# Kernel optimization log

Measured on AMD Instinct MI355X. Metric: run time of the kernel, lower is better.

The kernel has to match this reference:

```python
import jax, jax.numpy as jnp
import numpy as np

N = 100000   # nodes
D = 64       # input_dim
R = 16       # supprot (num relations)
NB = 8       # num_base
H = 128      # h_dim
E = 3200000  # edges (avg degree 32)


def setup_inputs() -> dict:
    key = jax.random.key(0)
    ks = jax.random.split(key, 7)
    vertex = jax.random.normal(ks[0], (N, D), dtype=jnp.float32)
    edge_src = jax.random.randint(ks[1], (E,), 0, N)
    edge_dst = jax.random.randint(ks[2], (E,), 0, N)
    edge_rel = jax.random.randint(ks[3], (E,), 0, R)
    edge_val = jax.random.uniform(ks[4], (E,), dtype=jnp.float32)
    W = jax.random.normal(ks[5], (D * NB, H), dtype=jnp.float32) * 0.05
    W_comp = jax.random.normal(ks[6], (R, NB), dtype=jnp.float32) * 0.3
    B = jnp.zeros((H,), dtype=jnp.float32)
    return {"vertex": vertex, "edge_val": edge_val, "W": W, "W_comp": W_comp,
            "B": B, "edge_src": edge_src, "edge_dst": edge_dst, "edge_rel": edge_rel}


def reference(vertex, edge_val, W, W_comp, B, edge_src, edge_dst, edge_rel):
    # per-relation spmm: supports[:, r*D:(r+1)*D] = A_r @ vertex (relation-major concat)
    msg = edge_val[:, None] * vertex[edge_src]              # [E, D]
    seg = edge_dst * R + edge_rel                            # combined (node, relation) segment
    supports = jax.ops.segment_sum(msg, seg, num_segments=N * R)  # [N*R, D]
    supports = supports.reshape(N, R * D)                    # [N, R*D]
    # basis decomposition (faithful to original reshape/permute ordering)
    Wr = W.reshape(NB, D, H).transpose(1, 0, 2)              # [D, NB, H]
    V = jnp.einsum('rb,dbh->drh', W_comp, Wr).reshape(D * R, H)  # [D*R, H]
    return supports @ V + B
```

## Files before the change

kernel.cpp:

```cpp
#include <hip/hip_runtime.h>
#include <hip/hip_bf16.h>
#include <stdint.h>

#define N_NODES 100000
#define DIM     64
#define NRELS   16
#define NBASE   8
#define HDIM    128
#define NEDGE   3200000
#define KDIM    1024

#define CBSH    8
#define CBN     256
#define NCB     391
#define BCAP    9216
#define SEGPB   (CBN * NRELS)
#define REC_PAD 256
#define NOFS_STRIDE 257

#define P1_BLOCKS 500
#define P1_EPT    25

#define PRO_VEFF_BLKS 512
#define PRO_VTXB_BLKS 12500
#define PRO_BLKS (PRO_VEFF_BLKS + PRO_VTXB_BLKS + 2)

typedef __attribute__((ext_vector_type(8))) short  short8;
typedef __attribute__((ext_vector_type(4))) float  f32x4;

#define OFF_VEFF  0u
#define OFF_VTXB  262144u
#define OFF_BCUR  13062144u
#define OFF_NOFS  13064192u
#define OFF_REC1  13473792u
#define REC_BYTES ((size_t)(NCB * BCAP + REC_PAD) * 8u)
#define OFF_REC2  (13473792u + REC_BYTES)
#define WS_NEED   (OFF_REC2 + REC_BYTES)

static __device__ __forceinline__ unsigned short f2bf(float x) {
    union { float f; unsigned u; } t; t.f = x;
    unsigned u = t.u;
    unsigned r = u + 0x7FFFu + ((u >> 16) & 1u);
    return (unsigned short)(r >> 16);
}

__global__ __launch_bounds__(256) void prologue(
        const float* __restrict__ W, const float* __restrict__ Wc,
        __hip_bfloat16* __restrict__ veff,
        const float* __restrict__ vert, unsigned* __restrict__ vb,
        int* __restrict__ bcur) {
    int b = blockIdx.x, t = threadIdx.x;
    if (b < PRO_VEFF_BLKS) {
        int idx = b * 256 + t;
        int c = idx >> 7;
        int h = idx & 127;
        float acc = 0.f;
#pragma unroll
        for (int bb = 0; bb < NBASE; ++bb)
            acc += Wc[(c & 15) * NBASE + bb] * W[(bb * DIM + (c >> 4)) * HDIM + h];
        int kt = c >> 5, ko = c & 31;
        int lane = ((ko >> 3) << 4) | (h & 15);
        int j = ko & 7;
        int hb = h >> 4;
        ((unsigned short*)veff)[(size_t)((kt * 8 + hb) * 64 + lane) * 8 + j] = f2bf(acc);
    } else if (b < PRO_VEFF_BLKS + PRO_VTXB_BLKS) {
        int i = (b - PRO_VEFF_BLKS) * 256 + t;
        float2 f = ((const float2*)vert)[i];
        unsigned r;
        asm("v_cvt_pk_bf16_f32 %0, %1, %2" : "=v"(r) : "v"(f.x), "v"(f.y));
        vb[i] = r;
    } else {
        int i = (b - PRO_VEFF_BLKS - PRO_VTXB_BLKS) * 256 + t;
        if (i < NCB) bcur[i] = i * BCAP;
    }
}

__global__ __launch_bounds__(256) void pass1_scatter(
        const int* __restrict__ esrc, const int* __restrict__ edst,
        const int* __restrict__ erel, const float* __restrict__ eval,
        int* __restrict__ bcur, uint2* __restrict__ recs1) {
    __shared__ int lcnt[NCB], lbase[NCB];
    int t = threadIdx.x;
    int base = blockIdx.x * (256 * P1_EPT);
    for (int i = t; i < NCB; i += 256) lcnt[i] = 0;
    __syncthreads();
#pragma unroll 5
    for (int k = 0; k < P1_EPT; ++k)
        atomicAdd(&lcnt[edst[base + k * 256 + t] >> CBSH], 1);
    __syncthreads();
    for (int i = t; i < NCB; i += 256) {
        int c = lcnt[i];
        if (c > 0) lbase[i] = atomicAdd(&bcur[i], c);
        lcnt[i] = 0;
    }
    __syncthreads();
#pragma unroll 5
    for (int k = 0; k < P1_EPT; ++k) {
        int e = base + k * 256 + t;
        int dst = edst[e];
        int cb = dst >> CBSH;
        int slot = atomicAdd(&lcnt[cb], 1);
        uint2 r;
        r.x = (unsigned)esrc[e] | ((unsigned)erel[e] << 17)
            | ((unsigned)(dst & (CBN - 1)) << 21);
        r.y = __float_as_uint(eval[e]);
        recs1[lbase[cb] + slot] = r;
    }
}

__global__ __launch_bounds__(256) void pass2_scatter(
        const uint2* __restrict__ recs1, const int* __restrict__ bcur,
        int* __restrict__ nofs, uint2* __restrict__ recs2) {
    __shared__ int cur[SEGPB];
    __shared__ int wsum[4];
    int t = threadIdx.x;
    int cb = blockIdx.x;
    int r0 = cb * BCAP;
    int r1 = bcur[cb];
    int rend = r0 + BCAP; if (r1 > rend) r1 = rend;
    for (int i = t; i < SEGPB; i += 256) cur[i] = 0;
    __syncthreads();
    for (int i = r0 + t; i < r1; i += 256) {
        unsigned rx = recs1[i].x;
        int lseg = (int)(((rx >> 21) & 255u) * 16u + ((rx >> 17) & 15u));
        atomicAdd(&cur[lseg], 1);
    }
    __syncthreads();
    int b0 = t * 16;
    int vals[16]; int tsum = 0;
#pragma unroll
    for (int k = 0; k < 16; ++k) { vals[k] = cur[b0 + k]; tsum += vals[k]; }
    int lane = t & 63, w = t >> 6;
    int x = tsum;
#pragma unroll
    for (int d = 1; d < 64; d <<= 1) { int y = __shfl_up(x, d); if (lane >= d) x += y; }
    if (lane == 63) wsum[w] = x;
    __syncthreads();
    int wadd = 0;
    for (int i = 0; i < w; ++i) wadd += wsum[i];
    int run = r0 + wadd + x - tsum;
    nofs[cb * NOFS_STRIDE + t] = run;
#pragma unroll
    for (int k = 0; k < 16; ++k) { cur[b0 + k] = run; run += vals[k]; }
    if (t == 255) nofs[cb * NOFS_STRIDE + 256] = run;
    __syncthreads();
    for (int i = r0 + t; i < r1; i += 256) {
        uint2 r = recs1[i];
        int lseg = (int)(((r.x >> 21) & 255u) * 16u + ((r.x >> 17) & 15u));
        int pos = atomicAdd(&cur[lseg], 1);
        recs2[pos] = r;
    }
}

__global__ __launch_bounds__(512, 4) void fused_agg_gemm(
        const unsigned short* __restrict__ vtxb, const uint2* __restrict__ recs,
        const int* __restrict__ nofs, const __hip_bfloat16* __restrict__ veff,
        const float* __restrict__ bias, float* __restrict__ out) {
    __shared__ __align__(16) unsigned char smem[33 * 2048];
    int t = threadIdx.x;
    int g = blockIdx.x;
    int w = t >> 6, lane = t & 63;
    int q = lane >> 4, p = lane & 15;
    int nloc = w * 4 + q;
    int n = g * 32 + nloc;

    for (int i = t; i < 33 * 2048 / 16; i += 512)
        ((uint4*)smem)[i] = make_uint4(0, 0, 0, 0);
    __syncthreads();

    int cbn = n >> CBSH, lo = n & (CBN - 1);
    int e0 = nofs[cbn * NOFS_STRIDE + lo];
    int e1 = nofs[cbn * NOFS_STRIDE + lo + 1];

    unsigned rowb2 = (unsigned)nloc * 2048u
                   + ((unsigned)(p * 8) ^ ((unsigned)(nloc & 7) << 4));
    unsigned scrb2 = 32u * 2048u + (unsigned)(p * 8);

    f32x4 acc = (f32x4)0.f;
    int currel = -1;
    const uint2* vtx2 = (const uint2*)vtxb;

    uint2 r0, r1, r2, r3, r4, r5, r6, r7;
    r0 = recs[e0 + 0]; r1 = recs[e0 + 1]; r2 = recs[e0 + 2]; r3 = recs[e0 + 3];
    r4 = recs[e0 + 4]; r5 = recs[e0 + 5]; r6 = recs[e0 + 6]; r7 = recs[e0 + 7];

    for (int base = e0; __any(base < e1); base += 8) {
        uint2 v0 = vtx2[(size_t)(r0.x & 0x1FFFFu) * 16 + p];
        uint2 v1 = vtx2[(size_t)(r1.x & 0x1FFFFu) * 16 + p];
        uint2 v2 = vtx2[(size_t)(r2.x & 0x1FFFFu) * 16 + p];
        uint2 v3 = vtx2[(size_t)(r3.x & 0x1FFFFu) * 16 + p];
        uint2 v4 = vtx2[(size_t)(r4.x & 0x1FFFFu) * 16 + p];
        uint2 v5 = vtx2[(size_t)(r5.x & 0x1FFFFu) * 16 + p];
        uint2 v6 = vtx2[(size_t)(r6.x & 0x1FFFFu) * 16 + p];
        uint2 v7 = vtx2[(size_t)(r7.x & 0x1FFFFu) * 16 + p];
        int nb = base + 8;
        uint2 n0 = recs[nb + 0], n1 = recs[nb + 1], n2 = recs[nb + 2], n3 = recs[nb + 3];
        uint2 n4 = recs[nb + 4], n5 = recs[nb + 5], n6 = recs[nb + 6], n7 = recs[nb + 7];

#define PROC(K, RK, VK)                                                       \
        {                                                                     \
            bool active = (base + (K)) < e1;                                  \
            int rel = (int)((RK.x >> 17) & 15u);                              \
            float val = active ? __uint_as_float(RK.y) : 0.f;                 \
            bool chg = (rel != currel) && active;                             \
            float f0 = __uint_as_float(VK.x << 16);                           \
            float f1 = __uint_as_float(VK.x & 0xFFFF0000u);                   \
            float f2 = __uint_as_float(VK.y << 16);                           \
            float f3 = __uint_as_float(VK.y & 0xFFFF0000u);                   \
            float t0 = chg ? 0.f : acc[0];                                    \
            float t1 = chg ? 0.f : acc[1];                                    \
            float t2 = chg ? 0.f : acc[2];                                    \
            float t3 = chg ? 0.f : acc[3];                                    \
            acc[0] = fmaf(val, f0, t0);                                       \
            acc[1] = fmaf(val, f1, t1);                                       \
            acc[2] = fmaf(val, f2, t2);                                       \
            acc[3] = fmaf(val, f3, t3);                                       \
            currel = active ? rel : currel;                                   \
            unsigned addr = (active ? rowb2 : scrb2) + ((unsigned)rel << 7);  \
            unsigned lo_, hi_;                                                \
            asm("v_cvt_pk_bf16_f32 %0, %1, %2" : "=v"(lo_)                    \
                : "v"(acc[0]), "v"(acc[1]));                                  \
            asm("v_cvt_pk_bf16_f32 %0, %1, %2" : "=v"(hi_)                    \
                : "v"(acc[2]), "v"(acc[3]));                                  \
            *(uint2*)(smem + addr) = make_uint2(lo_, hi_);                    \
        }
        PROC(0, r0, v0) PROC(1, r1, v1) PROC(2, r2, v2) PROC(3, r3, v3)
        PROC(4, r4, v4) PROC(5, r5, v5) PROC(6, r6, v6) PROC(7, r7, v7)
#undef PROC
        r0 = n0; r1 = n1; r2 = n2; r3 = n3;
        r4 = n4; r5 = n5; r6 = n6; r7 = n7;
    }
    __syncthreads();

    int l15 = lane & 15, lhi = lane >> 4;
    unsigned axor = (unsigned)((l15 & 7) << 4);
    f32x4 acc0 = (f32x4)0.f, acc1 = (f32x4)0.f;
#pragma unroll
    for (int kt = 0; kt < 32; ++kt) {
        short8 bf = ((const short8*)veff)[(size_t)(kt * 8 + w) * 64 + lane];
        unsigned cbo = (unsigned)(kt * 64 + lhi * 16);
        short8 a0 = *(const short8*)(smem + (((unsigned)l15 * 2048 + cbo) ^ axor));
        short8 a1 = *(const short8*)(smem + (((unsigned)(16 + l15) * 2048 + cbo) ^ axor));
        acc0 = __builtin_amdgcn_mfma_f32_16x16x32_bf16(a0, bf, acc0, 0, 0, 0);
        acc1 = __builtin_amdgcn_mfma_f32_16x16x32_bf16(a1, bf, acc1, 0, 0, 0);
    }
    int h = w * 16 + l15;
    float bv = bias[h];
#pragma unroll
    for (int j = 0; j < 4; ++j) {
        out[(size_t)(g * 32 + lhi * 4 + j) * HDIM + h]      = acc0[j] + bv;
        out[(size_t)(g * 32 + 16 + lhi * 4 + j) * HDIM + h] = acc1[j] + bv;
    }
}

__global__ __launch_bounds__(256) void build_veff_plain(
        const float* __restrict__ W, const float* __restrict__ Wc,
        float* __restrict__ veff) {
    int idx = blockIdx.x * 256 + threadIdx.x;
    int c = idx >> 7, h = idx & 127;
    float acc = 0.f;
#pragma unroll
    for (int b = 0; b < NBASE; ++b)
        acc += Wc[(c & 15) * NBASE + b] * W[(b * DIM + (c >> 4)) * HDIM + h];
    veff[c * HDIM + h] = acc;
}
__global__ __launch_bounds__(256) void init_out_bias(
        const float* __restrict__ bias, float* __restrict__ out) {
    int idx = blockIdx.x * 256 + threadIdx.x;
    if (idx < N_NODES * HDIM) out[idx] = bias[idx & 127];
}
__global__ __launch_bounds__(128) void edge_slow(
        const float* __restrict__ vertex, const float* __restrict__ eval,
        const int* __restrict__ esrc, const int* __restrict__ edst,
        const int* __restrict__ erel, const float* __restrict__ veff,
        float* __restrict__ out) {
    int e = blockIdx.x;
    int h = threadIdx.x;
    __shared__ float vrow[DIM];
    int src = esrc[e], dst = edst[e], rel = erel[e];
    float val = eval[e];
    if (h < DIM) vrow[h] = vertex[(size_t)src * DIM + h];
    __syncthreads();
    float acc = 0.f;
#pragma unroll 8
    for (int d = 0; d < DIM; ++d)
        acc += vrow[d] * veff[(rel * DIM + d) * HDIM + h];
    atomicAdd(out + (size_t)dst * HDIM + h, val * acc);
}

extern "C" void kernel_launch(void* const* d_in, const int* in_sizes, int n_in,
                              void* d_out, int out_size, void* d_ws, size_t ws_size,
                              hipStream_t stream) {
    const float* vertex   = (const float*)d_in[0];
    const float* edge_val = (const float*)d_in[1];
    const float* W        = (const float*)d_in[2];
    const float* W_comp   = (const float*)d_in[3];
    const float* B        = (const float*)d_in[4];
    const int*   edge_src = (const int*)d_in[5];
    const int*   edge_dst = (const int*)d_in[6];
    const int*   edge_rel = (const int*)d_in[7];
    float* out = (float*)d_out;

    if (ws_size >= WS_NEED) {
        __hip_bfloat16* veff = (__hip_bfloat16*)((char*)d_ws + OFF_VEFF);
        unsigned* vtxb = (unsigned*)((char*)d_ws + OFF_VTXB);
        int*   bcur  = (int*)((char*)d_ws + OFF_BCUR);
        int*   nofs  = (int*)((char*)d_ws + OFF_NOFS);
        uint2* recs1 = (uint2*)((char*)d_ws + OFF_REC1);
        uint2* recs2 = (uint2*)((char*)d_ws + OFF_REC2);

        prologue<<<PRO_BLKS, 256, 0, stream>>>(W, W_comp, veff, vertex, vtxb, bcur);
        pass1_scatter<<<P1_BLOCKS, 256, 0, stream>>>(
            edge_src, edge_dst, edge_rel, edge_val, bcur, recs1);
        pass2_scatter<<<NCB, 256, 0, stream>>>(recs1, bcur, nofs, recs2);
        fused_agg_gemm<<<N_NODES / 32, 512, 0, stream>>>(
            (const unsigned short*)vtxb, recs2, nofs, veff, B, out);
    } else {
        float* veff = (float*)d_ws;
        build_veff_plain<<<KDIM * HDIM / 256, 256, 0, stream>>>(W, W_comp, veff);
        init_out_bias<<<(N_NODES * HDIM + 255) / 256, 256, 0, stream>>>(B, out);
        edge_slow<<<NEDGE, 128, 0, stream>>>(
            vertex, edge_val, edge_src, edge_dst, edge_rel, veff, out);
    }
}
```

Measured before the change: 195.6 us.

## Merge prologue with edge bucketing pass and halve coarse bucket size

Folds the first edge scatter pass into the prologue kernel as extra blocks, so there is one fewer launch and the bucketing runs alongside the bf16 conversions. The bucket cursor is now zeroed with a memset and stores relative counts. Coarse buckets shrink from 256 to 128 nodes, which doubles the number of pass-2 blocks and halves the per-block shared segment table. The vertex gather index math switches to 32-bit. A risk is the tighter per-bucket capacity margin, and records beyond capacity are dropped.

```diff
diff --git a/kernel.cpp b/kernel.cpp
--- a/kernel.cpp
+++ b/kernel.cpp
@@ -10,28 +10,28 @@
 #define NEDGE   3200000
 #define KDIM    1024
 
-#define CBSH    8
-#define CBN     256
-#define NCB     391
-#define BCAP    9216
+#define CBSH    7
+#define CBN     128
+#define NCB     782
+#define BCAP    4800
 #define SEGPB   (CBN * NRELS)
 #define REC_PAD 256
-#define NOFS_STRIDE 257
+#define NOFS_STRIDE 129
 
 #define P1_BLOCKS 500
 #define P1_EPT    25
 
 #define PRO_VEFF_BLKS 512
 #define PRO_VTXB_BLKS 12500
-#define PRO_BLKS (PRO_VEFF_BLKS + PRO_VTXB_BLKS + 2)
+#define TOT_BLKS (P1_BLOCKS + PRO_VEFF_BLKS + PRO_VTXB_BLKS)
 
 typedef __attribute__((ext_vector_type(8))) short  short8;
 typedef __attribute__((ext_vector_type(4))) float  f32x4;
 
 #define OFF_VEFF  0u
 #define OFF_VTXB  262144u
-#define OFF_BCUR  13062144u
-#define OFF_NOFS  13064192u
+#define OFF_CUR   13062144u
+#define OFF_NOFS  13066240u
 #define OFF_REC1  13473792u
 #define REC_BYTES ((size_t)(NCB * BCAP + REC_PAD) * 8u)
 #define OFF_REC2  (13473792u + REC_BYTES)
@@ -44,14 +44,43 @@
     return (unsigned short)(r >> 16);
 }
 
-__global__ __launch_bounds__(256) void prologue(
+__global__ __launch_bounds__(256) void pro_pass1(
+        const int* __restrict__ esrc, const int* __restrict__ edst,
+        const int* __restrict__ erel, const float* __restrict__ eval,
+        int* __restrict__ cur, uint2* __restrict__ recs1,
         const float* __restrict__ W, const float* __restrict__ Wc,
         __hip_bfloat16* __restrict__ veff,
-        const float* __restrict__ vert, unsigned* __restrict__ vb,
-        int* __restrict__ bcur) {
+        const float* __restrict__ vert, unsigned* __restrict__ vb) {
+    __shared__ int lcnt[NCB], lbase[NCB];
     int b = blockIdx.x, t = threadIdx.x;
-    if (b < PRO_VEFF_BLKS) {
-        int idx = b * 256 + t;
+    if (b < P1_BLOCKS) {
+        int base = b * (256 * P1_EPT);
+        for (int i = t; i < NCB; i += 256) lcnt[i] = 0;
+        __syncthreads();
+#pragma unroll 5
+        for (int k = 0; k < P1_EPT; ++k)
+            atomicAdd(&lcnt[edst[base + k * 256 + t] >> CBSH], 1);
+        __syncthreads();
+        for (int i = t; i < NCB; i += 256) {
+            int c = lcnt[i];
+            if (c > 0) lbase[i] = i * BCAP + atomicAdd(&cur[i], c);
+            lcnt[i] = 0;
+        }
+        __syncthreads();
+#pragma unroll 5
+        for (int k = 0; k < P1_EPT; ++k) {
+            int e = base + k * 256 + t;
+            int dst = edst[e];
+            int cb = dst >> CBSH;
+            int slot = atomicAdd(&lcnt[cb], 1);
+            uint2 r;
+            r.x = (unsigned)esrc[e] | ((unsigned)erel[e] << 17)
+                | ((unsigned)(dst & (CBN - 1)) << 21);
+            r.y = __float_as_uint(eval[e]);
+            recs1[lbase[cb] + slot] = r;
+        }
+    } else if (b < P1_BLOCKS + PRO_VEFF_BLKS) {
+        int idx = (b - P1_BLOCKS) * 256 + t;
         int c = idx >> 7;
         int h = idx & 127;
         float acc = 0.f;
@@ -63,73 +92,37 @@
         int j = ko & 7;
         int hb = h >> 4;
         ((unsigned short*)veff)[(size_t)((kt * 8 + hb) * 64 + lane) * 8 + j] = f2bf(acc);
-    } else if (b < PRO_VEFF_BLKS + PRO_VTXB_BLKS) {
-        int i = (b - PRO_VEFF_BLKS) * 256 + t;
+    } else {
+        int i = (b - P1_BLOCKS - PRO_VEFF_BLKS) * 256 + t;
         float2 f = ((const float2*)vert)[i];
         unsigned r;
         asm("v_cvt_pk_bf16_f32 %0, %1, %2" : "=v"(r) : "v"(f.x), "v"(f.y));
         vb[i] = r;
-    } else {
-        int i = (b - PRO_VEFF_BLKS - PRO_VTXB_BLKS) * 256 + t;
-        if (i < NCB) bcur[i] = i * BCAP;
-    }
-}
-
-__global__ __launch_bounds__(256) void pass1_scatter(
-        const int* __restrict__ esrc, const int* __restrict__ edst,
-        const int* __restrict__ erel, const float* __restrict__ eval,
-        int* __restrict__ bcur, uint2* __restrict__ recs1) {
-    __shared__ int lcnt[NCB], lbase[NCB];
-    int t = threadIdx.x;
-    int base = blockIdx.x * (256 * P1_EPT);
-    for (int i = t; i < NCB; i += 256) lcnt[i] = 0;
-    __syncthreads();
-#pragma unroll 5
-    for (int k = 0; k < P1_EPT; ++k)
-        atomicAdd(&lcnt[edst[base + k * 256 + t] >> CBSH], 1);
-    __syncthreads();
-    for (int i = t; i < NCB; i += 256) {
-        int c = lcnt[i];
-        if (c > 0) lbase[i] = atomicAdd(&bcur[i], c);
-        lcnt[i] = 0;
-    }
-    __syncthreads();
-#pragma unroll 5
-    for (int k = 0; k < P1_EPT; ++k) {
-        int e = base + k * 256 + t;
-        int dst = edst[e];
-        int cb = dst >> CBSH;
-        int slot = atomicAdd(&lcnt[cb], 1);
-        uint2 r;
-        r.x = (unsigned)esrc[e] | ((unsigned)erel[e] << 17)
-            | ((unsigned)(dst & (CBN - 1)) << 21);
-        r.y = __float_as_uint(eval[e]);
-        recs1[lbase[cb] + slot] = r;
     }
 }
 
 __global__ __launch_bounds__(256) void pass2_scatter(
-        const uint2* __restrict__ recs1, const int* __restrict__ bcur,
+        const uint2* __restrict__ recs1, const int* __restrict__ cur,
         int* __restrict__ nofs, uint2* __restrict__ recs2) {
-    __shared__ int cur[SEGPB];
+    __shared__ int scur[SEGPB];
     __shared__ int wsum[4];
     int t = threadIdx.x;
     int cb = blockIdx.x;
     int r0 = cb * BCAP;
-    int r1 = bcur[cb];
-    int rend = r0 + BCAP; if (r1 > rend) r1 = rend;
-    for (int i = t; i < SEGPB; i += 256) cur[i] = 0;
+    int cnt = cur[cb]; if (cnt > BCAP) cnt = BCAP;
+    int r1 = r0 + cnt;
+    for (int i = t; i < SEGPB; i += 256) scur[i] = 0;
     __syncthreads();
     for (int i = r0 + t; i < r1; i += 256) {
         unsigned rx = recs1[i].x;
-        int lseg = (int)(((rx >> 21) & 255u) * 16u + ((rx >> 17) & 15u));
-        atomicAdd(&cur[lseg], 1);
-    }
-    __syncthreads();
-    int b0 = t * 16;
-    int vals[16]; int tsum = 0;
-#pragma unroll
-    for (int k = 0; k < 16; ++k) { vals[k] = cur[b0 + k]; tsum += vals[k]; }
+        int lseg = (int)(((rx >> 21) & 127u) * 16u + ((rx >> 17) & 15u));
+        atomicAdd(&scur[lseg], 1);
+    }
+    __syncthreads();
+    int b0 = t * 8;
+    int vals[8]; int tsum = 0;
+#pragma unroll
+    for (int k = 0; k < 8; ++k) { vals[k] = scur[b0 + k]; tsum += vals[k]; }
     int lane = t & 63, w = t >> 6;
     int x = tsum;
 #pragma unroll
@@ -137,17 +130,17 @@
     if (lane == 63) wsum[w] = x;
     __syncthreads();
     int wadd = 0;
-    for (int i = 0; i < w; ++i) wadd += wsum[i];
+    for (int i = 0; i < 4; ++i) if (i < w) wadd += wsum[i];
     int run = r0 + wadd + x - tsum;
-    nofs[cb * NOFS_STRIDE + t] = run;
-#pragma unroll
-    for (int k = 0; k < 16; ++k) { cur[b0 + k] = run; run += vals[k]; }
-    if (t == 255) nofs[cb * NOFS_STRIDE + 256] = run;
+    if ((t & 1) == 0) nofs[cb * NOFS_STRIDE + (t >> 1)] = run;
+#pragma unroll
+    for (int k = 0; k < 8; ++k) { scur[b0 + k] = run; run += vals[k]; }
+    if (t == 255) nofs[cb * NOFS_STRIDE + CBN] = run;
     __syncthreads();
     for (int i = r0 + t; i < r1; i += 256) {
         uint2 r = recs1[i];
-        int lseg = (int)(((r.x >> 21) & 255u) * 16u + ((r.x >> 17) & 15u));
-        int pos = atomicAdd(&cur[lseg], 1);
+        int lseg = (int)(((r.x >> 21) & 127u) * 16u + ((r.x >> 17) & 15u));
+        int pos = atomicAdd(&scur[lseg], 1);
         recs2[pos] = r;
     }
 }
@@ -179,20 +172,21 @@
     f32x4 acc = (f32x4)0.f;
     int currel = -1;
     const uint2* vtx2 = (const uint2*)vtxb;
+    unsigned up = (unsigned)p;
 
     uint2 r0, r1, r2, r3, r4, r5, r6, r7;
     r0 = recs[e0 + 0]; r1 = recs[e0 + 1]; r2 = recs[e0 + 2]; r3 = recs[e0 + 3];
     r4 = recs[e0 + 4]; r5 = recs[e0 + 5]; r6 = recs[e0 + 6]; r7 = recs[e0 + 7];
 
     for (int base = e0; __any(base < e1); base += 8) {
-        uint2 v0 = vtx2[(size_t)(r0.x & 0x1FFFFu) * 16 + p];
-        uint2 v1 = vtx2[(size_t)(r1.x & 0x1FFFFu) * 16 + p];
-        uint2 v2 = vtx2[(size_t)(r2.x & 0x1FFFFu) * 16 + p];
-        uint2 v3 = vtx2[(size_t)(r3.x & 0x1FFFFu) * 16 + p];
-        uint2 v4 = vtx2[(size_t)(r4.x & 0x1FFFFu) * 16 + p];
-        uint2 v5 = vtx2[(size_t)(r5.x & 0x1FFFFu) * 16 + p];
-        uint2 v6 = vtx2[(size_t)(r6.x & 0x1FFFFu) * 16 + p];
-        uint2 v7 = vtx2[(size_t)(r7.x & 0x1FFFFu) * 16 + p];
+        uint2 v0 = vtx2[(r0.x & 0x1FFFFu) * 16u + up];
+        uint2 v1 = vtx2[(r1.x & 0x1FFFFu) * 16u + up];
+        uint2 v2 = vtx2[(r2.x & 0x1FFFFu) * 16u + up];
+        uint2 v3 = vtx2[(r3.x & 0x1FFFFu) * 16u + up];
+        uint2 v4 = vtx2[(r4.x & 0x1FFFFu) * 16u + up];
+        uint2 v5 = vtx2[(r5.x & 0x1FFFFu) * 16u + up];
+        uint2 v6 = vtx2[(r6.x & 0x1FFFFu) * 16u + up];
+        uint2 v7 = vtx2[(r7.x & 0x1FFFFu) * 16u + up];
         int nb = base + 8;
         uint2 n0 = recs[nb + 0], n1 = recs[nb + 1], n2 = recs[nb + 2], n3 = recs[nb + 3];
         uint2 n4 = recs[nb + 4], n5 = recs[nb + 5], n6 = recs[nb + 6], n7 = recs[nb + 7];
@@ -304,15 +298,16 @@
     if (ws_size >= WS_NEED) {
         __hip_bfloat16* veff = (__hip_bfloat16*)((char*)d_ws + OFF_VEFF);
         unsigned* vtxb = (unsigned*)((char*)d_ws + OFF_VTXB);
-        int*   bcur  = (int*)((char*)d_ws + OFF_BCUR);
+        int*   cur   = (int*)((char*)d_ws + OFF_CUR);
         int*   nofs  = (int*)((char*)d_ws + OFF_NOFS);
         uint2* recs1 = (uint2*)((char*)d_ws + OFF_REC1);
         uint2* recs2 = (uint2*)((char*)d_ws + OFF_REC2);
 
-        prologue<<<PRO_BLKS, 256, 0, stream>>>(W, W_comp, veff, vertex, vtxb, bcur);
-        pass1_scatter<<<P1_BLOCKS, 256, 0, stream>>>(
-            edge_src, edge_dst, edge_rel, edge_val, bcur, recs1);
-        pass2_scatter<<<NCB, 256, 0, stream>>>(recs1, bcur, nofs, recs2);
+        hipMemsetAsync(cur, 0, NCB * sizeof(int), stream);
+        pro_pass1<<<TOT_BLKS, 256, 0, stream>>>(
+            edge_src, edge_dst, edge_rel, edge_val, cur, recs1,
+            W, W_comp, veff, vertex, vtxb);
+        pass2_scatter<<<NCB, 256, 0, stream>>>(recs1, cur, nofs, recs2);
         fused_agg_gemm<<<N_NODES / 32, 512, 0, stream>>>(
             (const unsigned short*)vtxb, recs2, nofs, veff, B, out);
     } else {
```

New measurement: 204.8 us. 4.7% more time.

## Stage block edge records in LDS and triple-buffer vertex gathers

Applied to the files above, without the earlier changes.

Each block now copies the edge records for its 32 nodes into shared memory in one cooperative load. A three-stage software pipeline then issues the vertex-row gathers through inline global_load asm with explicit vmcnt waits, so up to sixteen gathers stay in flight while earlier edges are accumulated. The aim is to hide gather latency and remove the dependent global record loads from the critical path. In exchange, LDS per block grows past 80KB, which likely cuts resident blocks per CU. Edge counts are also silently capped at the staging capacity, which could drop edges for unusually dense node groups.

```diff
diff --git a/kernel.cpp b/kernel.cpp
--- a/kernel.cpp
+++ b/kernel.cpp
@@ -25,8 +25,11 @@
 #define PRO_VTXB_BLKS 12500
 #define PRO_BLKS (PRO_VEFF_BLKS + PRO_VTXB_BLKS + 2)
 
+#define CAPB    1696
+
 typedef __attribute__((ext_vector_type(8))) short  short8;
 typedef __attribute__((ext_vector_type(4))) float  f32x4;
+typedef __attribute__((ext_vector_type(2))) unsigned u32x2;
 
 #define OFF_VEFF  0u
 #define OFF_VTXB  262144u
@@ -153,24 +156,34 @@
 }
 
 __global__ __launch_bounds__(512, 4) void fused_agg_gemm(
-        const unsigned short* __restrict__ vtxb, const uint2* __restrict__ recs,
+        const unsigned short* __restrict__ vtxb, const u32x2* __restrict__ recs,
         const int* __restrict__ nofs, const __hip_bfloat16* __restrict__ veff,
         const float* __restrict__ bias, float* __restrict__ out) {
-    __shared__ __align__(16) unsigned char smem[33 * 2048];
+    __shared__ __align__(16) unsigned char smem[67584 + CAPB * 8];
+    u32x2* lrec = (u32x2*)(smem + 67584);
     int t = threadIdx.x;
     int g = blockIdx.x;
     int w = t >> 6, lane = t & 63;
     int q = lane >> 4, p = lane & 15;
     int nloc = w * 4 + q;
-    int n = g * 32 + nloc;
-
-    for (int i = t; i < 33 * 2048 / 16; i += 512)
+
+    for (int i = t; i < 67584 / 16; i += 512)
         ((uint4*)smem)[i] = make_uint4(0, 0, 0, 0);
-    __syncthreads();
-
-    int cbn = n >> CBSH, lo = n & (CBN - 1);
-    int e0 = nofs[cbn * NOFS_STRIDE + lo];
-    int e1 = nofs[cbn * NOFS_STRIDE + lo + 1];
+
+    int cb_ = g >> 3;
+    int lo0 = (g & 7) * 32;
+    int start = nofs[cb_ * NOFS_STRIDE + lo0];
+    int cnt = nofs[cb_ * NOFS_STRIDE + lo0 + 32] - start;
+    if (cnt > CAPB - 64) cnt = CAPB - 64;
+    for (int i = t; i < cnt; i += 512) lrec[i] = recs[start + i];
+    if (t < 64) lrec[cnt + t] = (u32x2)(0u);
+    __syncthreads();
+
+    int le0q = nofs[cb_ * NOFS_STRIDE + lo0 + nloc] - start;
+    int le1q = nofs[cb_ * NOFS_STRIDE + lo0 + nloc + 1] - start;
+    if (le0q > cnt) le0q = cnt;
+    if (le1q > cnt) le1q = cnt;
+    int rem = le1q - le0q;
 
     unsigned rowb2 = (unsigned)nloc * 2048u
                    + ((unsigned)(p * 8) ^ ((unsigned)(nloc & 7) << 4));
@@ -178,58 +191,82 @@
 
     f32x4 acc = (f32x4)0.f;
     int currel = -1;
-    const uint2* vtx2 = (const uint2*)vtxb;
-
-    uint2 r0, r1, r2, r3, r4, r5, r6, r7;
-    r0 = recs[e0 + 0]; r1 = recs[e0 + 1]; r2 = recs[e0 + 2]; r3 = recs[e0 + 3];
-    r4 = recs[e0 + 4]; r5 = recs[e0 + 5]; r6 = recs[e0 + 6]; r7 = recs[e0 + 7];
-
-    for (int base = e0; __any(base < e1); base += 8) {
-        uint2 v0 = vtx2[(size_t)(r0.x & 0x1FFFFu) * 16 + p];
-        uint2 v1 = vtx2[(size_t)(r1.x & 0x1FFFFu) * 16 + p];
-        uint2 v2 = vtx2[(size_t)(r2.x & 0x1FFFFu) * 16 + p];
-        uint2 v3 = vtx2[(size_t)(r3.x & 0x1FFFFu) * 16 + p];
-        uint2 v4 = vtx2[(size_t)(r4.x & 0x1FFFFu) * 16 + p];
-        uint2 v5 = vtx2[(size_t)(r5.x & 0x1FFFFu) * 16 + p];
-        uint2 v6 = vtx2[(size_t)(r6.x & 0x1FFFFu) * 16 + p];
-        uint2 v7 = vtx2[(size_t)(r7.x & 0x1FFFFu) * 16 + p];
-        int nb = base + 8;
-        uint2 n0 = recs[nb + 0], n1 = recs[nb + 1], n2 = recs[nb + 2], n3 = recs[nb + 3];
-        uint2 n4 = recs[nb + 4], n5 = recs[nb + 5], n6 = recs[nb + 6], n7 = recs[nb + 7];
-
-#define PROC(K, RK, VK)                                                       \
-        {                                                                     \
-            bool active = (base + (K)) < e1;                                  \
-            int rel = (int)((RK.x >> 17) & 15u);                              \
-            float val = active ? __uint_as_float(RK.y) : 0.f;                 \
-            bool chg = (rel != currel) && active;                             \
-            float f0 = __uint_as_float(VK.x << 16);                           \
-            float f1 = __uint_as_float(VK.x & 0xFFFF0000u);                   \
-            float f2 = __uint_as_float(VK.y << 16);                           \
-            float f3 = __uint_as_float(VK.y & 0xFFFF0000u);                   \
-            float t0 = chg ? 0.f : acc[0];                                    \
-            float t1 = chg ? 0.f : acc[1];                                    \
-            float t2 = chg ? 0.f : acc[2];                                    \
-            float t3 = chg ? 0.f : acc[3];                                    \
-            acc[0] = fmaf(val, f0, t0);                                       \
-            acc[1] = fmaf(val, f1, t1);                                       \
-            acc[2] = fmaf(val, f2, t2);                                       \
-            acc[3] = fmaf(val, f3, t3);                                       \
-            currel = active ? rel : currel;                                   \
-            unsigned addr = (active ? rowb2 : scrb2) + ((unsigned)rel << 7);  \
-            unsigned lo_, hi_;                                                \
-            asm("v_cvt_pk_bf16_f32 %0, %1, %2" : "=v"(lo_)                    \
-                : "v"(acc[0]), "v"(acc[1]));                                  \
-            asm("v_cvt_pk_bf16_f32 %0, %1, %2" : "=v"(hi_)                    \
-                : "v"(acc[2]), "v"(acc[3]));                                  \
-            *(uint2*)(smem + addr) = make_uint2(lo_, hi_);                    \
-        }
-        PROC(0, r0, v0) PROC(1, r1, v1) PROC(2, r2, v2) PROC(3, r3, v3)
-        PROC(4, r4, v4) PROC(5, r5, v5) PROC(6, r6, v6) PROC(7, r7, v7)
-#undef PROC
-        r0 = n0; r1 = n1; r2 = n2; r3 = n3;
-        r4 = n4; r5 = n5; r6 = n6; r7 = n7;
-    }
+    const u32x2* vtx2 = (const u32x2*)vtxb;
+    unsigned up = (unsigned)p;
+
+    u32x2 R0[8], R1[8], R2[8];
+    u32x2 G0[8], G1[8], G2[8];
+
+#define LDREC(RP, OFF)                                                        \
+    {                                                                         \
+        _Pragma("unroll")                                                     \
+        for (int k = 0; k < 8; ++k) RP[k] = lrec[le0q + (OFF) + k];           \
+    }
+#define GISSUE(GI, RI)                                                        \
+    {                                                                         \
+        _Pragma("unroll")                                                     \
+        for (int k = 0; k < 8; ++k) {                                         \
+            const u32x2* ap = vtx2 + ((RI[k][0] & 0x1FFFFu) * 16u + up);      \
+            asm volatile("global_load_dwordx2 %0, %1, off"                    \
+                         : "=v"(GI[k]) : "v"(ap) : "memory");                 \
+        }                                                                     \
+    }
+#define VWAIT16                                                               \
+    asm volatile("s_waitcnt vmcnt(16)" ::: "memory");                         \
+    __builtin_amdgcn_sched_barrier(0);
+#define PROC1(K, RP, GP, OFF)                                                 \
+    {                                                                         \
+        bool active = ((OFF) + (K)) < rem;                                    \
+        u32x2 RK = RP[K];                                                     \
+        u32x2 VK = GP[K];                                                     \
+        int rel = (int)((RK[0] >> 17) & 15u);                                 \
+        float val = active ? __uint_as_float(RK[1]) : 0.f;                    \
+        bool chg = (rel != currel) && active;                                 \
+        float f0 = __uint_as_float(VK[0] << 16);                              \
+        float f1 = __uint_as_float(VK[0] & 0xFFFF0000u);                      \
+        float f2 = __uint_as_float(VK[1] << 16);                              \
+        float f3 = __uint_as_float(VK[1] & 0xFFFF0000u);                      \
+        float t0 = chg ? 0.f : acc[0];                                        \
+        float t1 = chg ? 0.f : acc[1];                                        \
+        float t2 = chg ? 0.f : acc[2];                                        \
+        float t3 = chg ? 0.f : acc[3];                                        \
+        acc[0] = fmaf(val, f0, t0);                                           \
+        acc[1] = fmaf(val, f1, t1);                                           \
+        acc[2] = fmaf(val, f2, t2);                                           \
+        acc[3] = fmaf(val, f3, t3);                                           \
+        currel = active ? rel : currel;                                       \
+        unsigned addr = (active ? rowb2 : scrb2) + ((unsigned)rel << 7);      \
+        unsigned lo_, hi_;                                                    \
+        asm("v_cvt_pk_bf16_f32 %0, %1, %2" : "=v"(lo_)                        \
+            : "v"(acc[0]), "v"(acc[1]));                                      \
+        asm("v_cvt_pk_bf16_f32 %0, %1, %2" : "=v"(hi_)                        \
+            : "v"(acc[2]), "v"(acc[3]));                                      \
+        *(uint2*)(smem + addr) = make_uint2(lo_, hi_);                        \
+    }
+#define PROC8(GP, RP, OFF)                                                    \
+    PROC1(0, RP, GP, OFF) PROC1(1, RP, GP, OFF) PROC1(2, RP, GP, OFF)         \
+    PROC1(3, RP, GP, OFF) PROC1(4, RP, GP, OFF) PROC1(5, RP, GP, OFF)         \
+    PROC1(6, RP, GP, OFF) PROC1(7, RP, GP, OFF)
+#define ITER(GP, RP, GI, RI, OFF)                                             \
+    GISSUE(GI, RI)                                                            \
+    VWAIT16                                                                   \
+    PROC8(GP, RP, OFF)                                                        \
+    LDREC(RP, (OFF) + 24)
+
+    LDREC(R0, 0) LDREC(R1, 8) LDREC(R2, 16)
+    GISSUE(G0, R0) GISSUE(G1, R1)
+
+    for (int off = 0; __any(off < rem); off += 24) {
+        ITER(G0, R0, G2, R2, off)
+        ITER(G1, R1, G0, R0, off + 8)
+        ITER(G2, R2, G1, R1, off + 16)
+    }
+#undef ITER
+#undef PROC8
+#undef PROC1
+#undef VWAIT16
+#undef GISSUE
+#undef LDREC
     __syncthreads();
 
     int l15 = lane & 15, lhi = lane >> 4;
@@ -314,7 +351,7 @@
             edge_src, edge_dst, edge_rel, edge_val, bcur, recs1);
         pass2_scatter<<<NCB, 256, 0, stream>>>(recs1, bcur, nofs, recs2);
         fused_agg_gemm<<<N_NODES / 32, 512, 0, stream>>>(
-            (const unsigned short*)vtxb, recs2, nofs, veff, B, out);
+            (const unsigned short*)vtxb, (const u32x2*)recs2, nofs, veff, B, out);
     } else {
         float* veff = (float*)d_ws;
         build_veff_plain<<<KDIM * HDIM / 256, 256, 0, stream>>>(W, W_comp, veff);
```

New measurement: 204.6 us. 4.6% more time.

## Split pass2 scatter into four node-quarter blocks per coarse bucket

Applied to the files above, without the earlier changes.

Pass2 now launches four blocks per coarse bucket. Each block handles one quarter of the 256 nodes, keeps a smaller shared counter array, and computes its base offset by counting records that belong to earlier quarters. The aim is more parallelism and occupancy for the counting-sort pass, since only 391 blocks ran before. In exchange, each block must read all records of the bucket twice, so global reads of recs1 go up fourfold.

```diff
diff --git a/kernel.cpp b/kernel.cpp
--- a/kernel.cpp
+++ b/kernel.cpp
@@ -14,7 +14,7 @@
 #define CBN     256
 #define NCB     391
 #define BCAP    9216
-#define SEGPB   (CBN * NRELS)
+#define QSEG    1024
 #define REC_PAD 256
 #define NOFS_STRIDE 257
 
@@ -111,44 +111,58 @@
 __global__ __launch_bounds__(256) void pass2_scatter(
         const uint2* __restrict__ recs1, const int* __restrict__ bcur,
         int* __restrict__ nofs, uint2* __restrict__ recs2) {
-    __shared__ int cur[SEGPB];
+    __shared__ int scur[QSEG];
     __shared__ int wsum[4];
+    __shared__ int priorsum[4];
     int t = threadIdx.x;
-    int cb = blockIdx.x;
+    int b = blockIdx.x;
+    int cb = b >> 2, qt = b & 3;
     int r0 = cb * BCAP;
     int r1 = bcur[cb];
     int rend = r0 + BCAP; if (r1 > rend) r1 = rend;
-    for (int i = t; i < SEGPB; i += 256) cur[i] = 0;
-    __syncthreads();
+    for (int i = t; i < QSEG; i += 256) scur[i] = 0;
+    if (t < 4) priorsum[t] = 0;
+    __syncthreads();
+    int prior = 0;
     for (int i = r0 + t; i < r1; i += 256) {
         unsigned rx = recs1[i].x;
-        int lseg = (int)(((rx >> 21) & 255u) * 16u + ((rx >> 17) & 15u));
-        atomicAdd(&cur[lseg], 1);
-    }
-    __syncthreads();
-    int b0 = t * 16;
-    int vals[16]; int tsum = 0;
-#pragma unroll
-    for (int k = 0; k < 16; ++k) { vals[k] = cur[b0 + k]; tsum += vals[k]; }
+        int node = (int)((rx >> 21) & 255u);
+        int q = node >> 6;
+        prior += (q < qt) ? 1 : 0;
+        if (q == qt)
+            atomicAdd(&scur[(node & 63) * 16 + (int)((rx >> 17) & 15u)], 1);
+    }
     int lane = t & 63, w = t >> 6;
+#pragma unroll
+    for (int d = 1; d < 64; d <<= 1) prior += __shfl_xor(prior, d);
+    if (lane == 0) priorsum[w] = prior;
+    __syncthreads();
+    int prior_total = priorsum[0] + priorsum[1] + priorsum[2] + priorsum[3];
+    int b0 = t * 4;
+    int vals[4]; int tsum = 0;
+#pragma unroll
+    for (int k = 0; k < 4; ++k) { vals[k] = scur[b0 + k]; tsum += vals[k]; }
     int x = tsum;
 #pragma unroll
     for (int d = 1; d < 64; d <<= 1) { int y = __shfl_up(x, d); if (lane >= d) x += y; }
     if (lane == 63) wsum[w] = x;
     __syncthreads();
     int wadd = 0;
-    for (int i = 0; i < w; ++i) wadd += wsum[i];
-    int run = r0 + wadd + x - tsum;
-    nofs[cb * NOFS_STRIDE + t] = run;
-#pragma unroll
-    for (int k = 0; k < 16; ++k) { cur[b0 + k] = run; run += vals[k]; }
-    if (t == 255) nofs[cb * NOFS_STRIDE + 256] = run;
+    for (int i = 0; i < 4; ++i) if (i < w) wadd += wsum[i];
+    int run = r0 + prior_total + wadd + x - tsum;
+    if ((b0 & 15) == 0) nofs[cb * NOFS_STRIDE + qt * 64 + (b0 >> 4)] = run;
+#pragma unroll
+    for (int k = 0; k < 4; ++k) { scur[b0 + k] = run; run += vals[k]; }
+    if (qt == 3 && t == 255) nofs[cb * NOFS_STRIDE + 256] = run;
     __syncthreads();
     for (int i = r0 + t; i < r1; i += 256) {
         uint2 r = recs1[i];
-        int lseg = (int)(((r.x >> 21) & 255u) * 16u + ((r.x >> 17) & 15u));
-        int pos = atomicAdd(&cur[lseg], 1);
-        recs2[pos] = r;
+        unsigned rx = r.x;
+        int node = (int)((rx >> 21) & 255u);
+        if ((node >> 6) == qt) {
+            int pos = atomicAdd(&scur[(node & 63) * 16 + (int)((rx >> 17) & 15u)], 1);
+            recs2[pos] = r;
+        }
     }
 }
 
@@ -312,7 +326,7 @@
         prologue<<<PRO_BLKS, 256, 0, stream>>>(W, W_comp, veff, vertex, vtxb, bcur);
         pass1_scatter<<<P1_BLOCKS, 256, 0, stream>>>(
             edge_src, edge_dst, edge_rel, edge_val, bcur, recs1);
-        pass2_scatter<<<NCB, 256, 0, stream>>>(recs1, bcur, nofs, recs2);
+        pass2_scatter<<<NCB * 4, 256, 0, stream>>>(recs1, bcur, nofs, recs2);
         fused_agg_gemm<<<N_NODES / 32, 512, 0, stream>>>(
             (const unsigned short*)vtxb, recs2, nofs, veff, B, out);
     } else {
```

Result: slower. 220.0 us (+12.5%).
